# Performance work log

Measured on AMD Instinct MI355X. Metric: run time of the kernel, lower is better.

Reference implementation:

```python
import jax, jax.numpy as jnp
import numpy as np

TEMP = 0.07
LAM = 0.1
S, Q, P, D = 128, 64, 64, 256


def _l2norm(x):
    # torch F.normalize(p=2, eps=1e-12)
    n = jnp.linalg.norm(x, axis=-1, keepdims=True)
    return x / jnp.maximum(n, 1e-12)


def setup_inputs() -> dict:
    key = jax.random.key(0)
    k1, k2, k3, k4 = jax.random.split(key, 4)
    return {
        "article_title_embedding": jax.random.normal(k1, (1, D), jnp.float32),
        "section_title_embeddings": jax.random.normal(k2, (S, D), jnp.float32),
        "question_embeddings": jax.random.normal(k3, (S, Q, D), jnp.float32),
        "sentence_embeddings": jax.random.normal(k4, (S, P, D), jnp.float32),
    }


def reference(article_title_embedding, section_title_embeddings,
              question_embeddings, sentence_embeddings):
    qn = _l2norm(question_embeddings)   # [S,Q,D]
    sn = _l2norm(sentence_embeddings)   # [S,P,D]
    sn_flat = sn.reshape(-1, sn.shape[-1])  # [S*P, D] all sentences in article
    N_e = sn_flat.shape[0]

    # --- qs_loss: question -> own-section sentences positive, other sections negative ---
    pos_sim = jnp.einsum('sqd,spd->sqp', qn, sn)          # [S,Q,P]
    pos = jnp.exp(pos_sim / TEMP)                          # [S,Q,P]
    all_sim = jnp.einsum('sqd,md->sqm', qn, sn_flat)      # [S,Q,S*P]
    total_exp = jnp.sum(jnp.exp(all_sim / TEMP), axis=-1)  # [S,Q]
    own_exp = jnp.sum(pos, axis=-1)                        # [S,Q]
    neg_sum_exp = total_exp - own_exp                      # sum over other sections

    term1 = -LAM * pos + neg_sum_exp[..., None] / (1.0 - LAM)
    term2 = jnp.exp(jnp.float32(-1.0 / TEMP)) * jnp.float32(N_e - 1)
    N_g = jnp.clip(jnp.maximum(term1, term2), 1e-8, None)
    qs_loss = jnp.sum(-jnp.log(pos / (pos + N_g)))

    # --- sq_loss: section title -> own-section questions positive ---
    stn = _l2norm(section_title_embeddings)                # [S,D]
    pos_q = jnp.exp(jnp.einsum('sd,sqd->sq', stn, qn) / TEMP)  # [S,Q]
    numerator = jnp.sum(pos_q, axis=-1)                    # [S]
    all_q = jnp.exp(jnp.einsum('sd,tqd->stq', stn, qn) / TEMP)  # [S,S,Q]
    denominator = jnp.sum(all_q, axis=(1, 2))              # numerator + negatives
    sq_loss = jnp.sum(-jnp.log(numerator / denominator))

    # --- at_loss: article title vs section titles (no negatives -> 0, kept faithful) ---
    an = _l2norm(article_title_embedding)                  # [1,D]
    at_num = jnp.sum(jnp.exp((an @ stn.T) / TEMP))
    at_loss = -jnp.log(at_num / at_num)

    return qs_loss + sq_loss + at_loss
```

## Files before the change

kernel.cpp:

```cpp
#include <hip/hip_runtime.h>
#include <math.h>

#define S_DIM 128
#define Q_DIM 64
#define P_DIM 64
#define D_DIM 256
#define NQ (S_DIM * Q_DIM)
#define NS (S_DIM * P_DIM)

typedef __attribute__((ext_vector_type(4))) float f32x4;
typedef __attribute__((ext_vector_type(8))) short bf16x8;
typedef __attribute__((ext_vector_type(8))) _Float16 f16x8;
typedef __attribute__((ext_vector_type(4))) _Float16 f16x4;

__device__ __forceinline__ unsigned short f2bf(float f) {
    unsigned int u = __float_as_uint(f);
    u = (u + 0x7fffu + ((u >> 16) & 1u)) >> 16;
    return (unsigned short)u;
}
__device__ __forceinline__ float bf2f(unsigned short h) {
    return __uint_as_float(((unsigned int)h) << 16);
}


__global__ __launch_bounds__(256) void normsplit_kernel(
    const float* __restrict__ qm, const float* __restrict__ sm,
    const float* __restrict__ st, float* __restrict__ zero_region,
    _Float16* __restrict__ qf, _Float16* __restrict__ sf, _Float16* __restrict__ stf,
    unsigned short* __restrict__ q_hi, unsigned short* __restrict__ q_lo,
    unsigned short* __restrict__ s_hi, unsigned short* __restrict__ s_lo) {
    if (blockIdx.x < 34) {
        int i = blockIdx.x * 256 + threadIdx.x;
        if (i < 8456) zero_region[i] = 0.0f;
    }
    int row = blockIdx.x * 4 + (threadIdx.x >> 6);
    int lane = threadIdx.x & 63;
    const float* src;
    _Float16* fdst;
    unsigned short *hi = nullptr, *lo = nullptr;
    int r;
    if (row < NQ) {
        r = row; src = qm + (size_t)r * D_DIM; fdst = qf + (size_t)r * D_DIM;
        hi = q_hi + (size_t)r * D_DIM; lo = q_lo + (size_t)r * D_DIM;
    } else if (row < NQ + NS) {
        r = row - NQ; src = sm + (size_t)r * D_DIM; fdst = sf + (size_t)r * D_DIM;
        hi = s_hi + (size_t)r * D_DIM; lo = s_lo + (size_t)r * D_DIM;
    } else if (row < NQ + NS + S_DIM) {
        r = row - NQ - NS; src = st + (size_t)r * D_DIM; fdst = stf + (size_t)r * D_DIM;
    } else return;

    float4 v = reinterpret_cast<const float4*>(src)[lane];
    float ss = v.x * v.x + v.y * v.y + v.z * v.z + v.w * v.w;
    #pragma unroll
    for (int off = 32; off; off >>= 1) ss += __shfl_xor(ss, off);
    float inv = 1.0f / fmaxf(sqrtf(ss), 1e-12f);

    const float CF = sqrtf((1.0f / 0.07f) * 1.44269504088896f);
    float sc = inv * CF;
    float x[4] = {v.x * sc, v.y * sc, v.z * sc, v.w * sc};

    f16x4 fv;
    #pragma unroll
    for (int e = 0; e < 4; e++) fv[e] = (_Float16)x[e];
    reinterpret_cast<f16x4*>(fdst)[lane] = fv;

    if (hi) {
        ushort4 h, l;
        unsigned short* hp = &h.x; unsigned short* lp = &l.x;
        #pragma unroll
        for (int e = 0; e < 4; e++) {
            unsigned short hh = f2bf(x[e]);
            hp[e] = hh;
            lp[e] = f2bf(x[e] - bf2f(hh));
        }
        reinterpret_cast<ushort4*>(hi)[lane] = h;
        reinterpret_cast<ushort4*>(lo)[lane] = l;
    }
}

__global__ __launch_bounds__(256, 2) void mfma_l2stream_kernel(
    const _Float16* __restrict__ qf, const _Float16* __restrict__ sf,
    const _Float16* __restrict__ stf,
    float* __restrict__ total_exp, float* __restrict__ den, float* __restrict__ num) {
    const int tid = threadIdx.x;
    const int w = tid >> 6, lane = tid & 63;
    const int lane15 = lane & 15, kg = lane >> 4;

    const bool cpass = (blockIdx.x < 32);
    const _Float16* A;
    const _Float16* B;
    int row0, colbase, nG;
    if (cpass) {
        const int idx = (int)blockIdx.x * 4 + w;
        A = stf; B = qf;
        row0 = (idx >> 6) * 64;
        colbase = (idx & 63) * 128;
        nG = 4;
    } else {
        const int b2 = (int)blockIdx.x - 32;
        A = qf; B = sf;
        const int panel = (b2 & 7) * 2 + (w & 1);
        const int rg = (b2 >> 3) * 2 + (w >> 1);
        row0 = rg * 64;
        colbase = panel * 512;
        nG = 16;
    }

    f16x8 af[4][8];
    {
        const _Float16* ap = A + (((size_t)(row0 + lane15)) << 8) + kg * 8;
        #pragma unroll
        for (int mb = 0; mb < 4; mb++)
            #pragma unroll
            for (int c = 0; c < 8; c++)
                af[mb][c] = *reinterpret_cast<const f16x8*>(ap + mb * 16 * 256 + c * 32);
    }

    float rs[4][4] = {{0.f}}, nm[4][4] = {{0.f}};
    #pragma unroll
    for (int mb = 0; mb < 4; mb++)
        #pragma unroll
        for (int j = 0; j < 4; j++) { rs[mb][j] = 0.f; nm[mb][j] = 0.f; }

    const _Float16* bp = B + (((size_t)(colbase + lane15)) << 8) + kg * 8;

    for (int ct = 0; ct < nG; ct++) {
        f32x4 acc[4][2];
        #pragma unroll
        for (int mb = 0; mb < 4; mb++) {
            acc[mb][0] = (f32x4){0.f, 0.f, 0.f, 0.f};
            acc[mb][1] = (f32x4){0.f, 0.f, 0.f, 0.f};
        }
        const _Float16* bpc = bp + (size_t)ct * 32 * 256;
        #pragma unroll
        for (int c = 0; c < 8; c++) {
            f16x8 bf0 = *reinterpret_cast<const f16x8*>(bpc + c * 32);
            f16x8 bf1 = *reinterpret_cast<const f16x8*>(bpc + 16 * 256 + c * 32);
            #pragma unroll
            for (int mb = 0; mb < 4; mb++) {
                acc[mb][0] = __builtin_amdgcn_mfma_f32_16x16x32_f16(af[mb][c], bf0, acc[mb][0], 0, 0, 0);
                acc[mb][1] = __builtin_amdgcn_mfma_f32_16x16x32_f16(af[mb][c], bf1, acc[mb][1], 0, 0, 0);
            }
        }
        #pragma unroll
        for (int mb = 0; mb < 4; mb++)
            #pragma unroll
            for (int j = 0; j < 4; j++) {
                float e0 = exp2f(acc[mb][0][j]);
                float e1 = exp2f(acc[mb][1][j]);
                rs[mb][j] += e0 + e1;
                if (cpass) {
                    const int grow = row0 + mb * 16 + kg * 4 + j;
                    const int c0 = colbase + ct * 32 + lane15;
                    if ((c0 >> 6) == grow) nm[mb][j] += e0;
                    if (((c0 + 16) >> 6) == grow) nm[mb][j] += e1;
                }
            }
    }

    #pragma unroll
    for (int mb = 0; mb < 4; mb++)
        #pragma unroll
        for (int j = 0; j < 4; j++) {
            float v = rs[mb][j], u = nm[mb][j];
            #pragma unroll
            for (int off = 1; off < 16; off <<= 1) {
                v += __shfl_xor(v, off);
                if (cpass) u += __shfl_xor(u, off);
            }
            if (lane15 == 0) {
                const int grow = row0 + mb * 16 + kg * 4 + j;
                if (cpass) {
                    atomicAdd(&den[grow], v);
                    atomicAdd(&num[grow], u);
                } else {
                    atomicAdd(&total_exp[grow], v);
                }
            }
        }
}

__global__ __launch_bounds__(128) void qs2_kernel(
    const unsigned short* __restrict__ q_hi, const unsigned short* __restrict__ q_lo,
    const unsigned short* __restrict__ s_hi, const unsigned short* __restrict__ s_lo,
    const float* __restrict__ total_exp, const float* __restrict__ den,
    const float* __restrict__ num, double* __restrict__ loss_acc,
    unsigned int* __restrict__ ticket, float* __restrict__ out) {
    const int s = blockIdx.x >> 1;
    const int tid = threadIdx.x;
    const int wid2 = ((blockIdx.x & 1) << 1) + (tid >> 6);
    const int lane = tid & 63;
    __shared__ double wsum[2];
    __shared__ float w2[2];
    __shared__ unsigned int winner_s;

    const int arow = s * 64 + wid2 * 16 + (lane & 15);
    const int koff = (lane >> 4) * 8;

    bf16x8 ah[8], al[8];
    #pragma unroll
    for (int k8 = 0; k8 < 8; k8++) {
        ah[k8] = *reinterpret_cast<const bf16x8*>(&q_hi[(size_t)arow * D_DIM + k8 * 32 + koff]);
        al[k8] = *reinterpret_cast<const bf16x8*>(&q_lo[(size_t)arow * D_DIM + k8 * 32 + koff]);
    }

    f32x4 acc[4];
    #pragma unroll
    for (int n = 0; n < 4; n++) acc[n] = (f32x4){0.f, 0.f, 0.f, 0.f};
    #pragma unroll
    for (int n = 0; n < 4; n++) {
        const int brow = s * 64 + n * 16 + (lane & 15);
        #pragma unroll
        for (int k8 = 0; k8 < 8; k8++) {
            bf16x8 bh = *reinterpret_cast<const bf16x8*>(&s_hi[(size_t)brow * D_DIM + k8 * 32 + koff]);
            bf16x8 bl = *reinterpret_cast<const bf16x8*>(&s_lo[(size_t)brow * D_DIM + k8 * 32 + koff]);
            acc[n] = __builtin_amdgcn_mfma_f32_16x16x32_bf16(ah[k8], bh, acc[n], 0, 0, 0);
            acc[n] = __builtin_amdgcn_mfma_f32_16x16x32_bf16(ah[k8], bl, acc[n], 0, 0, 0);
            acc[n] = __builtin_amdgcn_mfma_f32_16x16x32_bf16(al[k8], bh, acc[n], 0, 0, 0);
        }
    }

    const float term2 = expf(-1.0f / 0.07f) * (float)(NS - 1);
    double lacc = 0.0;
    #pragma unroll
    for (int j = 0; j < 4; j++) {
        float e[4];
        float part = 0.0f;
        #pragma unroll
        for (int n = 0; n < 4; n++) { e[n] = exp2f(acc[n][j]); part += e[n]; }
        #pragma unroll
        for (int off = 1; off < 16; off <<= 1) part += __shfl_xor(part, off);
        const int trow = s * 64 + wid2 * 16 + (lane >> 4) * 4 + j;
        const float neg = total_exp[trow] - part;
        #pragma unroll
        for (int n = 0; n < 4; n++) {
            float posv = e[n];
            float t1 = fmaf(-0.1f, posv, neg / 0.9f);
            float Ng = fmaxf(fmaxf(t1, term2), 1e-8f);
            lacc += (double)(-logf(posv / (posv + Ng)));
        }
    }
    #pragma unroll
    for (int off = 1; off < 64; off <<= 1) lacc += __shfl_xor(lacc, off);
    if (lane == 0) wsum[tid >> 6] = lacc;
    __syncthreads();
    if (tid == 0) {
        atomicAdd(loss_acc, wsum[0] + wsum[1]);
        __threadfence();
        winner_s = atomicAdd(ticket, 1u);
    }
    __syncthreads();
    if (winner_s == 255) {
        __threadfence();
        float l = -logf(num[tid] / den[tid]);
        #pragma unroll
        for (int off = 1; off < 64; off <<= 1) l += __shfl_xor(l, off);
        if ((tid & 63) == 0) w2[tid >> 6] = l;
        __syncthreads();
        if (tid == 0) out[0] = (float)(loss_acc[0] + (double)(w2[0] + w2[1]));
    }
}

extern "C" void kernel_launch(void* const* d_in, const int* in_sizes, int n_in,
                              void* d_out, int out_size, void* d_ws, size_t ws_size,
                              hipStream_t stream) {
    const float* st = (const float*)d_in[1];
    const float* qm = (const float*)d_in[2];
    const float* sm = (const float*)d_in[3];

    float* ws        = (float*)d_ws;
    float* total_exp = ws;
    float* den       = ws + 8192;
    float* num       = ws + 8320;
    double* loss_acc = (double*)(ws + 8448);
    unsigned int* ticket = (unsigned int*)(ws + 8452);
    _Float16* fbase = (_Float16*)(ws + 8704);
    _Float16* qf  = fbase;
    _Float16* sf  = fbase + 2097152;
    _Float16* stf = fbase + 4194304;
    unsigned short* b16 = (unsigned short*)fbase;
    unsigned short* q_hi = b16 + 4718592;
    unsigned short* q_lo = b16 + 6815744;
    unsigned short* s_hi = b16 + 8912896;
    unsigned short* s_lo = b16 + 11010048;
    float* out = (float*)d_out;

    hipLaunchKernelGGL(normsplit_kernel, dim3(4128), dim3(256), 0, stream,
                       qm, sm, st, ws, qf, sf, stf, q_hi, q_lo, s_hi, s_lo);
    hipLaunchKernelGGL(mfma_l2stream_kernel, dim3(544), dim3(256), 0, stream,
                       qf, sf, stf, total_exp, den, num);
    hipLaunchKernelGGL(qs2_kernel, dim3(256), dim3(128), 0, stream,
                       q_hi, q_lo, s_hi, s_lo, total_exp, den, num,
                       loss_acc, ticket, out);
}
```

Baseline: 184.1 us.

## Stage B tiles into LDS via async global_load_lds with double buffering

Previously each wave streamed its B operand straight from global/L2 into registers with no sharing. Now each block of 4 waves covers a 128x1024 tile and stages 64-column B tiles into double-buffered LDS using global_load_lds, so two waves share each B tile and the next tile's load overlaps the current MFMAs. The grid shrinks from 544 to 520 blocks because the section-title pass now uses 8 larger blocks. This adds 64KB of LDS per block, which may limit occupancy, plus a __syncthreads per iteration, and the LDS layout may cause bank conflicts.

```diff
diff --git a/kernel.cpp b/kernel.cpp
--- a/kernel.cpp
+++ b/kernel.cpp
@@ -20,6 +20,11 @@
 }
 __device__ __forceinline__ float bf2f(unsigned short h) {
     return __uint_as_float(((unsigned int)h) << 16);
+}
+__device__ __forceinline__ void gload_lds16(const void* g, void* l) {
+    __builtin_amdgcn_global_load_lds(
+        (const __attribute__((address_space(1))) void*)g,
+        (__attribute__((address_space(3))) void*)l, 16, 0, 0);
 }
 
 
@@ -78,37 +83,33 @@
     }
 }
 
-__global__ __launch_bounds__(256, 2) void mfma_l2stream_kernel(
+__global__ __launch_bounds__(256, 2) void mfma_stream_kernel(
     const _Float16* __restrict__ qf, const _Float16* __restrict__ sf,
     const _Float16* __restrict__ stf,
     float* __restrict__ total_exp, float* __restrict__ den, float* __restrict__ num) {
+    __shared__ __align__(16) char lds[2][32768];
     const int tid = threadIdx.x;
     const int w = tid >> 6, lane = tid & 63;
     const int lane15 = lane & 15, kg = lane >> 4;
-
-    const bool cpass = (blockIdx.x < 32);
+    const int wr = w >> 1, wc = w & 1;
+
+    const bool cpass = (blockIdx.x < 8);
     const _Float16* A;
     const _Float16* B;
-    int row0, colbase, nG;
+    int row0, colbase;
     if (cpass) {
-        const int idx = (int)blockIdx.x * 4 + w;
-        A = stf; B = qf;
-        row0 = (idx >> 6) * 64;
-        colbase = (idx & 63) * 128;
-        nG = 4;
+        A = stf; B = qf; row0 = 0;
+        colbase = (int)blockIdx.x * 1024;
     } else {
-        const int b2 = (int)blockIdx.x - 32;
+        const int b2 = (int)blockIdx.x - 8;
         A = qf; B = sf;
-        const int panel = (b2 & 7) * 2 + (w & 1);
-        const int rg = (b2 >> 3) * 2 + (w >> 1);
-        row0 = rg * 64;
-        colbase = panel * 512;
-        nG = 16;
+        row0 = (b2 >> 3) * 128;
+        colbase = (b2 & 7) * 1024;
     }
 
     f16x8 af[4][8];
     {
-        const _Float16* ap = A + (((size_t)(row0 + lane15)) << 8) + kg * 8;
+        const _Float16* ap = A + (((size_t)(row0 + wr * 64 + lane15)) << 8) + kg * 8;
         #pragma unroll
         for (int mb = 0; mb < 4; mb++)
             #pragma unroll
@@ -116,32 +117,46 @@
                 af[mb][c] = *reinterpret_cast<const f16x8*>(ap + mb * 16 * 256 + c * 32);
     }
 
-    float rs[4][4] = {{0.f}}, nm[4][4] = {{0.f}};
+    auto STAGE = [&](int buf, int t) {
+        const _Float16* src = B + (((size_t)(colbase + t * 64 + lane)) << 8) + w * 64;
+        #pragma unroll
+        for (int i = 0; i < 8; i++)
+            gload_lds16(src + i * 8, &lds[buf][0] + w * 8192 + i * 1024);
+    };
+
+    float rs[4][4], nm[4][4];
     #pragma unroll
     for (int mb = 0; mb < 4; mb++)
         #pragma unroll
         for (int j = 0; j < 4; j++) { rs[mb][j] = 0.f; nm[mb][j] = 0.f; }
 
-    const _Float16* bp = B + (((size_t)(colbase + lane15)) << 8) + kg * 8;
-
-    for (int ct = 0; ct < nG; ct++) {
+    STAGE(0, 0);
+    __syncthreads();
+
+    for (int t = 0; t < 16; t++) {
+        if (t + 1 < 16) STAGE((t + 1) & 1, t + 1);
+        const char* Bb = &lds[t & 1][0];
+
         f32x4 acc[4][2];
         #pragma unroll
         for (int mb = 0; mb < 4; mb++) {
             acc[mb][0] = (f32x4){0.f, 0.f, 0.f, 0.f};
             acc[mb][1] = (f32x4){0.f, 0.f, 0.f, 0.f};
         }
-        const _Float16* bpc = bp + (size_t)ct * 32 * 256;
+
         #pragma unroll
         for (int c = 0; c < 8; c++) {
-            f16x8 bf0 = *reinterpret_cast<const f16x8*>(bpc + c * 32);
-            f16x8 bf1 = *reinterpret_cast<const f16x8*>(bpc + 16 * 256 + c * 32);
+            f16x8 bf0 = *reinterpret_cast<const f16x8*>(
+                Bb + c * 4096 + kg * 1024 + (wc * 32 + lane15) * 16);
+            f16x8 bf1 = *reinterpret_cast<const f16x8*>(
+                Bb + c * 4096 + kg * 1024 + (wc * 32 + 16 + lane15) * 16);
             #pragma unroll
             for (int mb = 0; mb < 4; mb++) {
                 acc[mb][0] = __builtin_amdgcn_mfma_f32_16x16x32_f16(af[mb][c], bf0, acc[mb][0], 0, 0, 0);
                 acc[mb][1] = __builtin_amdgcn_mfma_f32_16x16x32_f16(af[mb][c], bf1, acc[mb][1], 0, 0, 0);
             }
         }
+
         #pragma unroll
         for (int mb = 0; mb < 4; mb++)
             #pragma unroll
@@ -150,12 +165,13 @@
                 float e1 = exp2f(acc[mb][1][j]);
                 rs[mb][j] += e0 + e1;
                 if (cpass) {
-                    const int grow = row0 + mb * 16 + kg * 4 + j;
-                    const int c0 = colbase + ct * 32 + lane15;
+                    const int grow = row0 + wr * 64 + mb * 16 + kg * 4 + j;
+                    const int c0 = colbase + t * 64 + wc * 32 + lane15;
                     if ((c0 >> 6) == grow) nm[mb][j] += e0;
                     if (((c0 + 16) >> 6) == grow) nm[mb][j] += e1;
                 }
             }
+        __syncthreads();
     }
 
     #pragma unroll
@@ -169,7 +185,7 @@
                 if (cpass) u += __shfl_xor(u, off);
             }
             if (lane15 == 0) {
-                const int grow = row0 + mb * 16 + kg * 4 + j;
+                const int grow = row0 + wr * 64 + mb * 16 + kg * 4 + j;
                 if (cpass) {
                     atomicAdd(&den[grow], v);
                     atomicAdd(&num[grow], u);
@@ -287,7 +303,7 @@
 
     hipLaunchKernelGGL(normsplit_kernel, dim3(4128), dim3(256), 0, stream,
                        qm, sm, st, ws, qf, sf, stf, q_hi, q_lo, s_hi, s_lo);
-    hipLaunchKernelGGL(mfma_l2stream_kernel, dim3(544), dim3(256), 0, stream,
+    hipLaunchKernelGGL(mfma_stream_kernel, dim3(520), dim3(256), 0, stream,
                        qf, sf, stf, total_exp, den, num);
     hipLaunchKernelGGL(qs2_kernel, dim3(256), dim3(128), 0, stream,
                        q_hi, q_lo, s_hi, s_lo, total_exp, den, num,
```

After: 178.9 us. -2.8%, faster.

## Store fp16 normalized embeddings in k-chunk-major layout for coalesced MFMA loads

Applied to the files above, without the earlier changes.

The normalize kernel now writes fp16 rows in a transposed layout grouped by 8-element k-chunks, [D/8][rows][8], so the MFMA kernel's fragment loads across lanes hit contiguous memory instead of rows strided by 512 bytes. The section-title pass is also remapped from 32 blocks covering 128 columns each to 8 blocks covering 1024 columns each. This shortens the grid from 544 to 520 blocks. The normalize kernel's scattered 8-byte stores become less coalesced in exchange.

```diff
diff --git a/kernel.cpp b/kernel.cpp
--- a/kernel.cpp
+++ b/kernel.cpp
@@ -26,7 +26,7 @@
 __global__ __launch_bounds__(256) void normsplit_kernel(
     const float* __restrict__ qm, const float* __restrict__ sm,
     const float* __restrict__ st, float* __restrict__ zero_region,
-    _Float16* __restrict__ qf, _Float16* __restrict__ sf, _Float16* __restrict__ stf,
+    _Float16* __restrict__ qft, _Float16* __restrict__ sft, _Float16* __restrict__ stft,
     unsigned short* __restrict__ q_hi, unsigned short* __restrict__ q_lo,
     unsigned short* __restrict__ s_hi, unsigned short* __restrict__ s_lo) {
     if (blockIdx.x < 34) {
@@ -36,17 +36,17 @@
     int row = blockIdx.x * 4 + (threadIdx.x >> 6);
     int lane = threadIdx.x & 63;
     const float* src;
-    _Float16* fdst;
+    _Float16* ft;
+    int NR, r;
     unsigned short *hi = nullptr, *lo = nullptr;
-    int r;
     if (row < NQ) {
-        r = row; src = qm + (size_t)r * D_DIM; fdst = qf + (size_t)r * D_DIM;
+        r = row; src = qm + (size_t)r * D_DIM; ft = qft; NR = NQ;
         hi = q_hi + (size_t)r * D_DIM; lo = q_lo + (size_t)r * D_DIM;
     } else if (row < NQ + NS) {
-        r = row - NQ; src = sm + (size_t)r * D_DIM; fdst = sf + (size_t)r * D_DIM;
+        r = row - NQ; src = sm + (size_t)r * D_DIM; ft = sft; NR = NS;
         hi = s_hi + (size_t)r * D_DIM; lo = s_lo + (size_t)r * D_DIM;
     } else if (row < NQ + NS + S_DIM) {
-        r = row - NQ - NS; src = st + (size_t)r * D_DIM; fdst = stf + (size_t)r * D_DIM;
+        r = row - NQ - NS; src = st + (size_t)r * D_DIM; ft = stft; NR = S_DIM;
     } else return;
 
     float4 v = reinterpret_cast<const float4*>(src)[lane];
@@ -62,7 +62,7 @@
     f16x4 fv;
     #pragma unroll
     for (int e = 0; e < 4; e++) fv[e] = (_Float16)x[e];
-    reinterpret_cast<f16x4*>(fdst)[lane] = fv;
+    *reinterpret_cast<f16x4*>(ft + ((size_t)(lane >> 1) * NR + r) * 8 + (lane & 1) * 4) = fv;
 
     if (hi) {
         ushort4 h, l;
@@ -78,64 +78,56 @@
     }
 }
 
-__global__ __launch_bounds__(256, 2) void mfma_l2stream_kernel(
-    const _Float16* __restrict__ qf, const _Float16* __restrict__ sf,
-    const _Float16* __restrict__ stf,
+__global__ __launch_bounds__(256, 2) void mfma_l2s_kernel(
+    const _Float16* __restrict__ qft, const _Float16* __restrict__ sft,
+    const _Float16* __restrict__ stft,
     float* __restrict__ total_exp, float* __restrict__ den, float* __restrict__ num) {
     const int tid = threadIdx.x;
     const int w = tid >> 6, lane = tid & 63;
     const int lane15 = lane & 15, kg = lane >> 4;
 
-    const bool cpass = (blockIdx.x < 32);
+    const bool cpass = (blockIdx.x < 8);
     const _Float16* A;
     const _Float16* B;
-    int row0, colbase, nG;
+    int row0, colbase, NRA;
     if (cpass) {
-        const int idx = (int)blockIdx.x * 4 + w;
-        A = stf; B = qf;
-        row0 = (idx >> 6) * 64;
-        colbase = (idx & 63) * 128;
-        nG = 4;
+        A = stft; B = qft; NRA = S_DIM;
+        row0 = (w >> 1) * 64;
+        colbase = (int)blockIdx.x * 1024 + (w & 1) * 512;
     } else {
-        const int b2 = (int)blockIdx.x - 32;
-        A = qf; B = sf;
-        const int panel = (b2 & 7) * 2 + (w & 1);
-        const int rg = (b2 >> 3) * 2 + (w >> 1);
-        row0 = rg * 64;
-        colbase = panel * 512;
-        nG = 16;
+        const int b2 = (int)blockIdx.x - 8;
+        A = qft; B = sft; NRA = NQ;
+        row0 = ((b2 >> 3) * 2 + (w >> 1)) * 64;
+        colbase = (b2 & 7) * 1024 + (w & 1) * 512;
     }
 
     f16x8 af[4][8];
-    {
-        const _Float16* ap = A + (((size_t)(row0 + lane15)) << 8) + kg * 8;
-        #pragma unroll
-        for (int mb = 0; mb < 4; mb++)
-            #pragma unroll
-            for (int c = 0; c < 8; c++)
-                af[mb][c] = *reinterpret_cast<const f16x8*>(ap + mb * 16 * 256 + c * 32);
-    }
-
-    float rs[4][4] = {{0.f}}, nm[4][4] = {{0.f}};
     #pragma unroll
     for (int mb = 0; mb < 4; mb++)
         #pragma unroll
+        for (int c = 0; c < 8; c++)
+            af[mb][c] = *reinterpret_cast<const f16x8*>(
+                A + ((size_t)(c * 4 + kg) * NRA + row0 + mb * 16 + lane15) * 8);
+
+    float rs[4][4], nm[4][4];
+    #pragma unroll
+    for (int mb = 0; mb < 4; mb++)
+        #pragma unroll
         for (int j = 0; j < 4; j++) { rs[mb][j] = 0.f; nm[mb][j] = 0.f; }
 
-    const _Float16* bp = B + (((size_t)(colbase + lane15)) << 8) + kg * 8;
-
-    for (int ct = 0; ct < nG; ct++) {
+    for (int cg = 0; cg < 16; cg++) {
+        const int c0 = colbase + cg * 32;
         f32x4 acc[4][2];
         #pragma unroll
         for (int mb = 0; mb < 4; mb++) {
             acc[mb][0] = (f32x4){0.f, 0.f, 0.f, 0.f};
             acc[mb][1] = (f32x4){0.f, 0.f, 0.f, 0.f};
         }
-        const _Float16* bpc = bp + (size_t)ct * 32 * 256;
         #pragma unroll
         for (int c = 0; c < 8; c++) {
-            f16x8 bf0 = *reinterpret_cast<const f16x8*>(bpc + c * 32);
-            f16x8 bf1 = *reinterpret_cast<const f16x8*>(bpc + 16 * 256 + c * 32);
+            const _Float16* p = B + ((size_t)(c * 4 + kg) * 8192 + c0 + lane15) * 8;
+            f16x8 bf0 = *reinterpret_cast<const f16x8*>(p);
+            f16x8 bf1 = *reinterpret_cast<const f16x8*>(p + 16 * 8);
             #pragma unroll
             for (int mb = 0; mb < 4; mb++) {
                 acc[mb][0] = __builtin_amdgcn_mfma_f32_16x16x32_f16(af[mb][c], bf0, acc[mb][0], 0, 0, 0);
@@ -151,9 +143,9 @@
                 rs[mb][j] += e0 + e1;
                 if (cpass) {
                     const int grow = row0 + mb * 16 + kg * 4 + j;
-                    const int c0 = colbase + ct * 32 + lane15;
-                    if ((c0 >> 6) == grow) nm[mb][j] += e0;
-                    if (((c0 + 16) >> 6) == grow) nm[mb][j] += e1;
+                    const int cc = c0 + lane15;
+                    if ((cc >> 6) == grow) nm[mb][j] += e0;
+                    if (((cc + 16) >> 6) == grow) nm[mb][j] += e1;
                 }
             }
     }
@@ -275,9 +267,9 @@
     double* loss_acc = (double*)(ws + 8448);
     unsigned int* ticket = (unsigned int*)(ws + 8452);
     _Float16* fbase = (_Float16*)(ws + 8704);
-    _Float16* qf  = fbase;
-    _Float16* sf  = fbase + 2097152;
-    _Float16* stf = fbase + 4194304;
+    _Float16* qft  = fbase;
+    _Float16* sft  = fbase + 2097152;
+    _Float16* stft = fbase + 4194304;
     unsigned short* b16 = (unsigned short*)fbase;
     unsigned short* q_hi = b16 + 4718592;
     unsigned short* q_lo = b16 + 6815744;
@@ -286,9 +278,9 @@
     float* out = (float*)d_out;
 
     hipLaunchKernelGGL(normsplit_kernel, dim3(4128), dim3(256), 0, stream,
-                       qm, sm, st, ws, qf, sf, stf, q_hi, q_lo, s_hi, s_lo);
-    hipLaunchKernelGGL(mfma_l2stream_kernel, dim3(544), dim3(256), 0, stream,
-                       qf, sf, stf, total_exp, den, num);
+                       qm, sm, st, ws, qft, sft, stft, q_hi, q_lo, s_hi, s_lo);
+    hipLaunchKernelGGL(mfma_l2s_kernel, dim3(520), dim3(256), 0, stream,
+                       qft, sft, stft, total_exp, den, num);
     hipLaunchKernelGGL(qs2_kernel, dim3(256), dim3(128), 0, stream,
                        q_hi, q_lo, s_hi, s_lo, total_exp, den, num,
                        loss_acc, ticket, out);
```

New measurement: 174.6 us. 5.2% less time.
